# Kernel optimization log

Measured on AMD Instinct MI355X. Metric: run time of the kernel, lower is better.

The kernel has to match this reference:

```python
import jax, jax.numpy as jnp
import numpy as np

B, C, H, W = 16, 256, 64, 64
K = 3
K2 = K * K
EPS = 1e-5


def setup_inputs() -> dict:
    key = jax.random.key(0)
    ks = jax.random.split(key, 5)
    scale_r = 1.0 / np.sqrt(C)
    return {
        "X": jax.random.normal(ks[0], (B, C, H, W), dtype=jnp.float32),
        "w_reduce": jax.random.normal(ks[1], (C, C), dtype=jnp.float32) * scale_r,
        "b_reduce": jax.random.normal(ks[2], (C,), dtype=jnp.float32) * 0.01,
        "gamma": jnp.ones((C,), dtype=jnp.float32),
        "beta": jnp.zeros((C,), dtype=jnp.float32),
        "w_span": jax.random.normal(ks[3], (C * K2, C), dtype=jnp.float32) * scale_r,
        "b_span": jax.random.normal(ks[4], (C * K2,), dtype=jnp.float32) * 0.01,
    }


def _unfold3x3(X):
    # torch nn.Unfold(3, padding=1, stride=1): patches (B, C, 9, H, W),
    # kernel positions row-major, channel slowest -- matches torch ordering.
    b, c, h, w = X.shape
    Xp = jnp.pad(X, ((0, 0), (0, 0), (1, 1), (1, 1)))
    return jnp.stack(
        [Xp[:, :, i:i + h, j:j + w] for i in range(K) for j in range(K)], axis=2
    )  # (B, C, 9, H, W)


def reference(X, w_reduce, b_reduce, gamma, beta, w_span, b_span):
    # stride=1 -> AvgPool is Identity. reduce: 1x1 conv C -> C (reduction=1)
    Wr = jnp.einsum('bchw,oc->bohw', X, w_reduce) + b_reduce[None, :, None, None]
    # BatchNorm2d (training mode: biased batch stats over B,H,W) + ReLU
    mean = Wr.mean(axis=(0, 2, 3))
    var = Wr.var(axis=(0, 2, 3))
    Wn = (Wr - mean[None, :, None, None]) * jax.lax.rsqrt(var[None, :, None, None] + EPS)
    Wn = jax.nn.relu(Wn * gamma[None, :, None, None] + beta[None, :, None, None])
    # span: 1x1 conv C -> g*k^2 (g = C since group_ch = 1)
    Ker = jnp.einsum('bchw,oc->bohw', Wn, w_span) + b_span[None, :, None, None]
    Ker = Ker.reshape(B, C, K2, H * W)  # (b, g, k^2, h*w); group_ch broadcast dim implied
    patches = _unfold3x3(X).reshape(B, C, K2, H * W)
    out = (patches * Ker).sum(axis=2)  # fused multiply-reduce over k^2
    return out.reshape(B, C, H, W)
```

## Files before the change

kernel.cpp:

```cpp
#include <hip/hip_runtime.h>
#include <stdint.h>


typedef __attribute__((ext_vector_type(4))) float f32x4;
typedef __attribute__((ext_vector_type(8))) short s16x8;
typedef __attribute__((ext_vector_type(8))) __bf16 bf16x8;

#define WAITV(N) asm volatile("s_waitcnt vmcnt(" #N ")" ::: "memory")
#define WAITL0   asm volatile("s_waitcnt lgkmcnt(0)" ::: "memory")
#define PIN()    asm volatile("" ::: "memory")
#define BAR()    do { PIN(); __builtin_amdgcn_s_barrier(); PIN(); } while (0)

__device__ __forceinline__ float bf2f(uint16_t u){
  union { uint32_t i; float f; } v; v.i = ((uint32_t)u) << 16; return v.f;
}
__device__ __forceinline__ uint16_t f2bf(float f){
  __bf16 h = (__bf16)f;
  return __builtin_bit_cast(uint16_t, h);
}

template <typename V>
__device__ __forceinline__ auto mfma16x16x32(V a, V b, f32x4 c, int)
    -> decltype(__builtin_amdgcn_mfma_f32_16x16x32_bf16(a, b, c, 0, 0, 0)) {
  return __builtin_amdgcn_mfma_f32_16x16x32_bf16(a, b, c, 0, 0, 0);
}
template <typename V>
__device__ __forceinline__ f32x4 mfma16x16x32(V a, V b, f32x4 c, long) {
  bf16x8 aa = __builtin_bit_cast(bf16x8, a);
  bf16x8 bb = __builtin_bit_cast(bf16x8, b);
  return __builtin_amdgcn_mfma_f32_16x16x32_bf16(aa, bb, c, 0, 0, 0);
}

typedef uint32_t u32_g __attribute__((address_space(1)));
typedef uint32_t u32_l __attribute__((address_space(3)));
__device__ __forceinline__ void glds16(const void* g, void* l){
  __builtin_amdgcn_global_load_lds((const u32_g*)g, (u32_l*)l, 16, 0, 0);
}

__global__ __launch_bounds__(256) void prep_weights(
    const float* __restrict__ wred, const float* __restrict__ wsp,
    uint16_t* __restrict__ wrt, uint16_t* __restrict__ wspt){
  int id = blockIdx.x * 256 + threadIdx.x;
  union { uint4 v; uint16_t h[8]; } u;
  if (id < 8192){
    int ks = id >> 10;
    int o  = (id >> 2) & 255;
    int j0 = (id & 3) * 8;
    const float* s = wred + o * 256 + ks * 32 + j0;
    #pragma unroll
    for (int i = 0; i < 8; i++) u.h[i] = f2bf(s[i]);
    *(uint4*)(wrt + ((size_t)(ks * 256 + o) * 32 + j0)) = u.v;
  } else {
    int c16 = id - 8192;
    int j0  = (c16 & 3) * 8;
    int row = c16 >> 2;
    int phys = row % 144;
    int mtks = row / 144;
    int mt = mtks & 15, ks = mtks >> 4;
    int g = phys & 15, k2 = phys >> 4;
    int sg = mt * 144 + g * 9 + k2;
    const float* s = wsp + (size_t)sg * 256 + ks * 32 + j0;
    #pragma unroll
    for (int i = 0; i < 8; i++) u.h[i] = f2bf(s[i]);
    *(uint4*)(wspt + ((size_t)row * 32 + j0)) = u.v;
  }
}

__global__ __launch_bounds__(256) void k1_reduce_gemm(
    const float* __restrict__ X, const uint16_t* __restrict__ wrt,
    const float* __restrict__ bred, uint16_t* __restrict__ Wr,
    float* __restrict__ part){
  const int pt = blockIdx.x, mt = blockIdx.y, b = blockIdx.z;
  const int p0 = pt * 128, o0 = mt * 128;
  __shared__ __align__(16) uint16_t Al[2][128*32];
  __shared__ __align__(16) uint16_t Bl[2][128*32];
  __shared__ float redS[256], redQ[256];
  const int t = threadIdx.x;
  const int wv = t >> 6, lane = t & 63, q = lane >> 4, l = lane & 15;
  const int wm = wv >> 1, wn = wv & 1;
  const int c2 = (t & 15) * 2, seg = t >> 4;
  f32x4 acc[4][4] = {};
  union { float f[8]; float4 v[2]; } v0, v1;

  auto stageA = [&](int ks, int buf){
    const char* src = (const char*)(wrt + ((size_t)ks * 256 + o0) * 32);
    char* dst = (char*)(&Al[buf][0]);
    for (int cc = wv; cc < 8; cc += 4)
      glds16(src + cc*1024 + lane*16, dst + cc*1024);
  };
  auto loadB = [&](int ks){
    const float* s0 = X + ((size_t)(b * 256 + ks * 32 + c2)) * 4096 + p0 + seg * 8;
    const float* s1 = s0 + 4096;
    v0.v[0] = *(const float4*)(s0 + 0);
    v0.v[1] = *(const float4*)(s0 + 4);
    v1.v[0] = *(const float4*)(s1 + 0);
    v1.v[1] = *(const float4*)(s1 + 4);
  };
  auto writeB = [&](int buf){
    uint16_t* dst = &Bl[buf][(seg * 8) * 32 + c2];
    #pragma unroll
    for (int i = 0; i < 8; i++){
      uint32_t pk = (uint32_t)f2bf(v0.f[i]) | ((uint32_t)f2bf(v1.f[i]) << 16);
      *(uint32_t*)(dst + (size_t)i * 32) = pk;
    }
  };

  stageA(0, 0); loadB(0); writeB(0);
  __syncthreads();
  int cur = 0;
  for (int ks = 0; ks < 8; ks++){
    if (ks < 7){ stageA(ks + 1, cur ^ 1); loadB(ks + 1); }
    s16x8 af[4], bfv[4];
    #pragma unroll
    for (int mi = 0; mi < 4; mi++)
      af[mi] = *(const s16x8*)(&Al[cur][(wm*64 + mi*16 + l)*32 + q*8]);
    #pragma unroll
    for (int ni = 0; ni < 4; ni++)
      bfv[ni] = *(const s16x8*)(&Bl[cur][(wn*64 + ni*16 + l)*32 + q*8]);
    #pragma unroll
    for (int mi = 0; mi < 4; mi++)
      #pragma unroll
      for (int ni = 0; ni < 4; ni++)
        acc[mi][ni] = mfma16x16x32(af[mi], bfv[ni], acc[mi][ni], 0);
    if (ks < 7) writeB(cur ^ 1);
    __syncthreads();
    cur ^= 1;
  }
  float ssum[4][4] = {}, ssq[4][4] = {};
  #pragma unroll
  for (int mi = 0; mi < 4; mi++){
    int o = o0 + wm*64 + mi*16 + q*4;
    float4 br = *(const float4*)(bred + o);
    int slab = o >> 5, orem = o & 31;
    #pragma unroll
    for (int ni = 0; ni < 4; ni++){
      int p = p0 + wn*64 + ni*16 + l;
      f32x4 v = acc[mi][ni];
      float e0 = v[0] + br.x, e1 = v[1] + br.y, e2 = v[2] + br.z, e3 = v[3] + br.w;
      ssum[mi][0] += e0; ssq[mi][0] += e0*e0;
      ssum[mi][1] += e1; ssq[mi][1] += e1*e1;
      ssum[mi][2] += e2; ssq[mi][2] += e2*e2;
      ssum[mi][3] += e3; ssq[mi][3] += e3*e3;
      uint32_t lo = (uint32_t)f2bf(e0) | ((uint32_t)f2bf(e1) << 16);
      uint32_t hi = (uint32_t)f2bf(e2) | ((uint32_t)f2bf(e3) << 16);
      uint2 pk; pk.x = lo; pk.y = hi;
      *(uint2*)(Wr + ((size_t)((b*8 + slab)*4096 + p)) * 32 + orem) = pk;
    }
  }
  #pragma unroll
  for (int mi = 0; mi < 4; mi++)
    #pragma unroll
    for (int j = 0; j < 4; j++){
      #pragma unroll
      for (int off = 1; off < 16; off <<= 1){
        ssum[mi][j] += __shfl_xor(ssum[mi][j], off);
        ssq[mi][j]  += __shfl_xor(ssq[mi][j],  off);
      }
    }
  if (l == 0){
    #pragma unroll
    for (int mi = 0; mi < 4; mi++)
      #pragma unroll
      for (int j = 0; j < 4; j++){
        int ch_local = wm*64 + mi*16 + q*4 + j;
        redS[ch_local*2 + wn] = ssum[mi][j];
        redQ[ch_local*2 + wn] = ssq[mi][j];
      }
  }
  __syncthreads();
  {
    int ch_local = t >> 1, m = t & 1;
    float val = m ? (redQ[ch_local*2] + redQ[ch_local*2+1])
                  : (redS[ch_local*2] + redS[ch_local*2+1]);
    int ch = o0 + ch_local;
    int idx = pt*16 + b;
    part[((size_t)ch*512 + idx)*2 + m] = val;
  }
}

__global__ __launch_bounds__(64) void bn_final(
    const float* __restrict__ part, const float* __restrict__ gamma,
    const float* __restrict__ beta, float* __restrict__ coeffs){
  int c = blockIdx.x, t = threadIdx.x;
  float s = 0.f, sq = 0.f;
  const float* p = part + (size_t)c * 1024;
  #pragma unroll
  for (int i = 0; i < 8; i++){
    float2 v = *(const float2*)(p + (t*8 + i)*2);
    s += v.x; sq += v.y;
  }
  #pragma unroll
  for (int off = 1; off < 64; off <<= 1){
    s  += __shfl_xor(s,  off);
    sq += __shfl_xor(sq, off);
  }
  if (t == 0){
    const float inv = 1.0f / 65536.0f;
    float mean = s * inv;
    float var  = sq * inv - mean * mean;
    float rstd = rsqrtf(var + 1e-5f);
    float A = gamma[c] * rstd;
    float Bc = beta[c] - mean * A;
    coeffs[2*c] = A; coeffs[2*c+1] = Bc;
  }
}

__global__ __launch_bounds__(256) void bn_apply(uint16_t* __restrict__ Wr,
                                                const float* __restrict__ coeffs){
  __shared__ float cf[512];
  cf[threadIdx.x]       = coeffs[threadIdx.x];
  cf[threadIdx.x + 256] = coeffs[threadIdx.x + 256];
  __syncthreads();
  #pragma unroll
  for (int it = 0; it < 4; it++){
    size_t c16 = (size_t)blockIdx.x * 256 + threadIdx.x + (size_t)it * (2048u*256u);
    uint16_t* pch = Wr + c16 * 8;
    int sj = (int)((c16 >> 14) & 7);
    int j0 = (int)(c16 & 3) * 8;
    union { uint4 v; uint16_t h[8]; } u;
    u.v = *(const uint4*)pch;
    #pragma unroll
    for (int i = 0; i < 8; i++){
      int cch = sj * 32 + j0 + i;
      float v = bf2f(u.h[i]);
      v = fmaf(v, cf[2*cch], cf[2*cch+1]);
      v = fmaxf(v, 0.f);
      u.h[i] = f2bf(v);
    }
    *(uint4*)pch = u.v;
  }
}

__global__ __launch_bounds__(256, 2) void k3_span_inv(
    const uint16_t* __restrict__ Wn, const uint16_t* __restrict__ wspt,
    const float* __restrict__ bspan, const float* __restrict__ X,
    float* __restrict__ out){
  const int orig = blockIdx.x;
  const int wgid = (orig & 7) * 512 + (orig >> 3);
  const int mt = wgid & 15, pt = (wgid >> 4) & 15, b = wgid >> 8;
  const int p0 = pt * 256;
  __shared__ __align__(16) uint16_t Al[3][144*32];
  __shared__ __align__(16) float Xl[16*412];
  __shared__ float bsp[144];
  const int t = threadIdx.x;
  const int wv = t >> 6, lane = t & 63, q = lane >> 4, l = lane & 15;
  const int qs = q ^ ((l >> 1) & 3);
  if (t < 144){
    int g = t & 15, k2 = t >> 4;
    bsp[t] = bspan[mt*144 + g*9 + k2];
  }
  if (t < 192){
    int ch = t / 12, rr = t % 12, r = rr >> 1;
    Xl[ch*412 + r*68 + (rr & 1)*65] = 0.f;
  }
  PIN();
  f32x4 acc[9][4] = {};

  const int lsw = ((lane >> 2) << 6) + ((((lane & 3) ^ ((lane >> 3) & 3))) << 4);
  const char* Abase = (const char*)(wspt + (size_t)mt * (144*32));
  const size_t AslabB = (size_t)16 * 144 * 64;
  const uint16_t* Bb = Wn + (((size_t)(b*8))*4096 + p0 + wv*64 + l)*32 + q*8;
  const size_t BslabE = (size_t)4096 * 32;

  auto stageA = [&](int ks, int buf){
    const char* asrc = Abase + (size_t)ks * AslabB + lsw;
    char* adst = (char*)(&Al[buf][0]);
    glds16(asrc + (size_t)wv*1024,     adst + wv*1024);
    glds16(asrc + (size_t)(wv+4)*1024, adst + (wv+4)*1024);
    if (wv == 0) glds16(asrc + 8*1024, adst + 8*1024);
  };

  s16x8 bb[2][4];
  float4 xv[6];
  stageA(0, 0);
  PIN();
  #pragma unroll
  for (int ni = 0; ni < 4; ni++) bb[0][ni] = *(const s16x8*)(Bb + 0*BslabE + (size_t)ni*512);
  #pragma unroll
  for (int ni = 0; ni < 4; ni++) bb[1][ni] = *(const s16x8*)(Bb + 1*BslabE + (size_t)ni*512);
  PIN();
  stageA(1, 1);
  PIN();
  if (wv == 0) { WAITV(7); } else { WAITV(6); }
  WAITL0;
  BAR();

  #pragma unroll
  for (int ks = 0; ks < 8; ks++){
    if (ks < 6) stageA(ks + 2, (ks + 2) % 3);
    PIN();
    if (ks == 0){
      #pragma unroll
      for (int i = 0; i < 6; i++){
        int v = t + i*256;
        int ch = v / 96, rem = v - ch*96;
        int r = rem >> 4, c4 = (rem & 15) * 4;
        int hr = pt*4 - 1 + r;
        int hrc = min(max(hr, 0), 63);
        xv[i] = *(const float4*)(X + ((size_t)(b*256 + mt*16 + ch))*4096 + hrc*64 + c4);
      }
      PIN();
    }
    if (ks == 1){
      #pragma unroll
      for (int i = 0; i < 6; i++){
        int v = t + i*256;
        int ch = v / 96, rem = v - ch*96;
        int r = rem >> 4, c4 = (rem & 15) * 4;
        int hr = pt*4 - 1 + r;
        bool ok = (hr >= 0) && (hr < 64);
        float4 val = xv[i];
        int d = ch*412 + r*68 + 1 + c4;
        Xl[d]   = ok ? val.x : 0.f;
        Xl[d+1] = ok ? val.y : 0.f;
        Xl[d+2] = ok ? val.z : 0.f;
        Xl[d+3] = ok ? val.w : 0.f;
      }
      PIN();
    }
    __builtin_amdgcn_s_setprio(1);
    #pragma unroll
    for (int mi = 0; mi < 9; mi++){
      s16x8 af = *(const s16x8*)(&Al[ks % 3][(mi*16 + l)*32 + qs*8]);
      acc[mi][0] = mfma16x16x32(bb[ks & 1][0], af, acc[mi][0], 0);
      acc[mi][1] = mfma16x16x32(bb[ks & 1][1], af, acc[mi][1], 0);
      acc[mi][2] = mfma16x16x32(bb[ks & 1][2], af, acc[mi][2], 0);
      acc[mi][3] = mfma16x16x32(bb[ks & 1][3], af, acc[mi][3], 0);
    }
    __builtin_amdgcn_s_setprio(0);
    if (ks < 6){
      #pragma unroll
      for (int ni = 0; ni < 4; ni++)
        bb[ks & 1][ni] = *(const s16x8*)(Bb + (size_t)(ks+2)*BslabE + (size_t)ni*512);
    }
    if (ks < 7){
      if (ks == 0){
        if (wv == 0) { WAITV(13); } else { WAITV(12); }
      } else if (ks < 6){
        if (wv == 0) { WAITV(7); } else { WAITV(6); }
      } else {
        WAITV(0);
      }
      WAITL0;
      BAR();
    }
  }

  float bs[9];
  #pragma unroll
  for (int k2 = 0; k2 < 9; k2++) bs[k2] = bsp[k2*16 + l];
  #pragma unroll
  for (int k2 = 0; k2 < 9; k2++)
    #pragma unroll
    for (int ni = 0; ni < 4; ni++){
      acc[k2][ni][0] += bs[k2]; acc[k2][ni][1] += bs[k2];
      acc[k2][ni][2] += bs[k2]; acc[k2][ni][3] += bs[k2];
    }
  const int h = pt*4 + wv;
  const int gg = mt*16 + l;
  float* Oc = out + ((size_t)(b*256 + gg) * 64 + h) * 64;
  const float* Xrow = &Xl[l*412 + wv*68];
  #pragma unroll
  for (int ni = 0; ni < 4; ni++){
    f32x4 res = {0.f, 0.f, 0.f, 0.f};
    #pragma unroll
    for (int dh = 0; dh < 3; dh++){
      const float* xp = Xrow + dh*68 + ni*16 + q*4;
      f32x4 xa = *(const f32x4*)xp;
      float2 xb = *(const float2*)(xp + 4);
      float x[6] = {xa[0], xa[1], xa[2], xa[3], xb.x, xb.y};
      #pragma unroll
      for (int dw = 0; dw < 3; dw++){
        const int k2 = dh*3 + dw;
        #pragma unroll
        for (int reg = 0; reg < 4; reg++)
          res[reg] = fmaf(acc[k2][ni][reg], x[reg + dw], res[reg]);
      }
    }
    *(f32x4*)(Oc + ni*16 + q*4) = res;
  }
}

extern "C" void kernel_launch(void* const* d_in, const int* in_sizes, int n_in,
                              void* d_out, int out_size, void* d_ws, size_t ws_size,
                              hipStream_t stream) {
  const float* X     = (const float*)d_in[0];
  const float* wred  = (const float*)d_in[1];
  const float* bred  = (const float*)d_in[2];
  const float* gamma = (const float*)d_in[3];
  const float* beta  = (const float*)d_in[4];
  const float* wsp   = (const float*)d_in[5];
  const float* bsp   = (const float*)d_in[6];
  float* out = (float*)d_out;

  char* ws = (char*)d_ws;
  uint16_t* Wr   = (uint16_t*)(ws);
  uint16_t* wrt  = (uint16_t*)(ws + 33554432);
  uint16_t* wspt = (uint16_t*)(ws + 33554432 + 131072);
  float* part    = (float*)(ws + 33554432 + 131072 + 1179648);
  float* coeffs  = (float*)(ws + 33554432 + 131072 + 1179648 + 1048576);
  if (ws_size < (size_t)(33554432 + 131072 + 1179648 + 1048576 + 2048)) return;

  prep_weights<<<320, 256, 0, stream>>>(wred, wsp, wrt, wspt);
  k1_reduce_gemm<<<dim3(32, 2, 16), 256, 0, stream>>>(X, wrt, bred, Wr, part);
  bn_final<<<256, 64, 0, stream>>>(part, gamma, beta, coeffs);
  bn_apply<<<2048, 256, 0, stream>>>(Wr, coeffs);
  k3_span_inv<<<4096, 256, 0, stream>>>(Wr, wspt, bsp, X, out);
}
```

Measured before the change: 134.3 us.

## Deepen A-tile LDS ring to four buffers and prefetch A fragments into registers

The weight-tile LDS ring grows from three to four buffers, with three slabs staged up front. The A fragments for the next k-step are now read from LDS into registers while the current step's MFMAs run, so LDS reads overlap the matrix math. The wait and barrier schedule is rewritten to match the deeper pipeline. The cost is more LDS per block, nine extra vector registers per thread, and fragile hand-written vmcnt counts. With launch bounds of two blocks per SM these could reduce occupancy or cause a race if the counts are wrong.

```diff
diff --git a/kernel.cpp b/kernel.cpp
--- a/kernel.cpp
+++ b/kernel.cpp
@@ -239,7 +239,7 @@
   const int wgid = (orig & 7) * 512 + (orig >> 3);
   const int mt = wgid & 15, pt = (wgid >> 4) & 15, b = wgid >> 8;
   const int p0 = pt * 256;
-  __shared__ __align__(16) uint16_t Al[3][144*32];
+  __shared__ __align__(16) uint16_t Al[4][144*32];
   __shared__ __align__(16) float Xl[16*412];
   __shared__ float bsp[144];
   const int t = threadIdx.x;
@@ -271,24 +271,26 @@
   };
 
   s16x8 bb[2][4];
+  s16x8 afr[9];
   float4 xv[6];
   stageA(0, 0);
+  stageA(1, 1);
+  stageA(2, 2);
   PIN();
   #pragma unroll
   for (int ni = 0; ni < 4; ni++) bb[0][ni] = *(const s16x8*)(Bb + 0*BslabE + (size_t)ni*512);
   #pragma unroll
   for (int ni = 0; ni < 4; ni++) bb[1][ni] = *(const s16x8*)(Bb + 1*BslabE + (size_t)ni*512);
   PIN();
-  stageA(1, 1);
-  PIN();
-  if (wv == 0) { WAITV(7); } else { WAITV(6); }
-  WAITL0;
+  WAITV(8);
   BAR();
+  #pragma unroll
+  for (int mi = 0; mi < 9; mi++)
+    afr[mi] = *(const s16x8*)(&Al[0][(mi*16 + l)*32 + qs*8]);
 
   #pragma unroll
   for (int ks = 0; ks < 8; ks++){
-    if (ks < 6) stageA(ks + 2, (ks + 2) % 3);
-    PIN();
+    if (ks < 5){ stageA(ks + 3, (ks + 3) & 3); PIN(); }
     if (ks == 0){
       #pragma unroll
       for (int i = 0; i < 6; i++){
@@ -321,11 +323,13 @@
     __builtin_amdgcn_s_setprio(1);
     #pragma unroll
     for (int mi = 0; mi < 9; mi++){
-      s16x8 af = *(const s16x8*)(&Al[ks % 3][(mi*16 + l)*32 + qs*8]);
-      acc[mi][0] = mfma16x16x32(bb[ks & 1][0], af, acc[mi][0], 0);
-      acc[mi][1] = mfma16x16x32(bb[ks & 1][1], af, acc[mi][1], 0);
-      acc[mi][2] = mfma16x16x32(bb[ks & 1][2], af, acc[mi][2], 0);
-      acc[mi][3] = mfma16x16x32(bb[ks & 1][3], af, acc[mi][3], 0);
+      s16x8 cur = afr[mi];
+      if (ks < 7)
+        afr[mi] = *(const s16x8*)(&Al[(ks+1) & 3][(mi*16 + l)*32 + qs*8]);
+      acc[mi][0] = mfma16x16x32(bb[ks & 1][0], cur, acc[mi][0], 0);
+      acc[mi][1] = mfma16x16x32(bb[ks & 1][1], cur, acc[mi][1], 0);
+      acc[mi][2] = mfma16x16x32(bb[ks & 1][2], cur, acc[mi][2], 0);
+      acc[mi][3] = mfma16x16x32(bb[ks & 1][3], cur, acc[mi][3], 0);
     }
     __builtin_amdgcn_s_setprio(0);
     if (ks < 6){
@@ -333,15 +337,17 @@
       for (int ni = 0; ni < 4; ni++)
         bb[ks & 1][ni] = *(const s16x8*)(Bb + (size_t)(ks+2)*BslabE + (size_t)ni*512);
     }
-    if (ks < 7){
-      if (ks == 0){
-        if (wv == 0) { WAITV(13); } else { WAITV(12); }
-      } else if (ks < 6){
-        if (wv == 0) { WAITV(7); } else { WAITV(6); }
-      } else {
-        WAITV(0);
-      }
+    if (ks == 0){
+      BAR();
+    } else if (ks == 1){
+      if (wv == 0) { WAITV(7); } else { WAITV(6); }
       WAITL0;
+      BAR();
+    } else if (ks < 5){
+      if (wv == 0) { WAITV(7); } else { WAITV(6); }
+      BAR();
+    } else if (ks == 5){
+      WAITV(4);
       BAR();
     }
   }
```

New measurement: 149.8 us. +11.6%, slower.
